# Kernel tuning notes

Measured on AMD Instinct MI355X. Metric: run time of the kernel, lower is better.

The kernel has to match this reference:

```python
import jax, jax.numpy as jnp
import numpy as np

H = 256      # hidden_dim
NH = 8       # num_heads
D = H // NH  # per-head dim
NEG = -(2.0**32) + 1.0
EPS = 1e-5


def setup_inputs() -> dict:
    key = jax.random.key(0)
    ks = jax.random.split(key, 12)
    N, Tq, Tk = 2, 2048, 2048
    s = 1.0 / np.sqrt(H)
    return {
        "Q": jax.random.normal(ks[0], (N, Tq, H), jnp.float32),
        "K": jax.random.normal(ks[1], (N, Tk, H), jnp.float32),
        "V": jax.random.normal(ks[2], (N, Tk, H), jnp.float32),
        "Wq": jax.random.normal(ks[3], (H, H), jnp.float32) * s,
        "bq": jnp.zeros((H,), jnp.float32),
        "Wk": jax.random.normal(ks[4], (H, H), jnp.float32) * s,
        "bk": jnp.zeros((H,), jnp.float32),
        "Wv": jax.random.normal(ks[5], (H, H), jnp.float32) * s,
        "bv": jnp.zeros((H,), jnp.float32),
        "gamma": jnp.ones((H,), jnp.float32),
        "beta": jnp.zeros((H,), jnp.float32),
    }


def _split_heads(x):
    # [N,T,H] -> [h,N,T,D]  (matches torch split(dim=2)+cat(dim=0): head-major)
    N, T, _ = x.shape
    return x.reshape(N, T, NH, D).transpose(2, 0, 1, 3)


def reference(Q, K, V, Wq, bq, Wk, bk, Wv, bv, gamma, beta):
    N, Tq, _ = Q.shape
    Tk = K.shape[1]
    Ql = jax.nn.relu(Q @ Wq + bq)
    Kl = jax.nn.relu(K @ Wk + bk)
    Vl = jax.nn.relu(V @ Wv + bv)
    Qh, Kh, Vh = _split_heads(Ql), _split_heads(Kl), _split_heads(Vl)

    scores = jnp.einsum("hnqd,hnkd->hnqk", Qh, Kh) / jnp.sqrt(jnp.float32(D))
    key_mask = jnp.sign(jnp.abs(K).sum(-1))    # [N,Tk]
    scores = jnp.where(key_mask[None, :, None, :] == 0, NEG, scores)
    attn = jax.nn.softmax(scores / 0.01, axis=-1)
    query_mask = jnp.sign(jnp.abs(Q).sum(-1))  # [N,Tq]
    attn = attn * query_mask[None, :, :, None]  # dropout p=0 -> identity

    ctx = jnp.einsum("hnqk,hnkd->hnqd", attn[..., :-1], Vh[:, :, :-1, :])
    out = ctx.transpose(1, 2, 0, 3).reshape(N, Tq, H)

    mu = out.mean(-1, keepdims=True)
    var = ((out - mu) ** 2).mean(-1, keepdims=True)
    out = (out - mu) / jnp.sqrt(var + EPS) * gamma + beta

    weight = attn.transpose(1, 2, 0, 3).reshape(N, Tq, NH * Tk).mean(-1)
    return out, weight
```

## Files before the change

kernel.cpp:

```cpp
#include <hip/hip_runtime.h>
#include <math.h>

#define H_DIM 256
#define NHEAD 8
#define DHEAD 32
#define NB 2
#define TSEQ 2048
#define LN_EPS 1e-5f

#define QK2_SCALE 25.503486f
#define SPLIT 4
#define TILES_PER (TSEQ / 64 / SPLIT)

typedef _Float16 half8 __attribute__((ext_vector_type(8)));
typedef _Float16 half4t __attribute__((ext_vector_type(4)));
typedef _Float16 half2t __attribute__((ext_vector_type(2)));
typedef float f32x4 __attribute__((ext_vector_type(4)));

__device__ __forceinline__ f32x4 mfma16(half8 a, half8 b, f32x4 c) {
  return __builtin_amdgcn_mfma_f32_16x16x32_f16(a, b, c, 0, 0, 0);
}
__device__ __forceinline__ float exp2fast(float x) {
  return __builtin_amdgcn_exp2f(x);
}
__device__ __forceinline__ half2t pkrtz(float a, float b) {
  return __builtin_bit_cast(half2t, __builtin_amdgcn_cvt_pkrtz(a, b));
}

__global__ __launch_bounds__(256) void mask_kernel(
    const float* __restrict__ Q, const float* __restrict__ K,
    float* __restrict__ qmask, float* __restrict__ kmask) {
  const int wid = threadIdx.x >> 6, lane = threadIdx.x & 63;
  int row = blockIdx.x * 4 + wid;
  const int total_q = NB * TSEQ;
  const float* src;
  float* dst;
  if (row < total_q) { src = Q + (size_t)row * H_DIM; dst = qmask + row; }
  else               { src = K + (size_t)(row - total_q) * H_DIM; dst = kmask + (row - total_q); }
  float4 v = *(const float4*)(src + lane * 4);
  float s = fabsf(v.x) + fabsf(v.y) + fabsf(v.z) + fabsf(v.w);
  #pragma unroll
  for (int off = 32; off > 0; off >>= 1) s += __shfl_xor(s, off);
  if (lane == 0) *dst = (s != 0.0f) ? 1.0f : 0.0f;
}

__global__ __launch_bounds__(256) void prepack_kernel(
    const float* __restrict__ Wq, const float* __restrict__ Wk, const float* __restrict__ Wv,
    const float* __restrict__ kmask,
    half8* __restrict__ WpkHi, half8* __restrict__ WpkLo, half8* __restrict__ AmaskF) {
  if (blockIdx.x >= 96) {
    int slot2 = (blockIdx.x - 96) * 256 + threadIdx.x;
    int n = slot2 >> 12;
    int rem = slot2 & 4095;
    int tile = rem >> 7;
    int c = (rem >> 6) & 1;
    int lane = rem & 63;
    int quad = lane >> 4, l15 = lane & 15;
    half8 am;
    #pragma unroll
    for (int j = 0; j < 8; ++j)
      am[j] = (l15 == 0) ? (_Float16)kmask[(size_t)n * TSEQ + tile * 64 + c * 32 + quad * 8 + j]
                         : (_Float16)0.0f;
    AmaskF[(((size_t)n * 32 + tile) * 2 + c) * 64 + lane] = am;
    return;
  }
  int slot = blockIdx.x * 256 + threadIdx.x;
  int lane = slot & 63;
  int fg = (slot >> 6) & 15;
  int s  = (slot >> 10) & 7;
  int which = slot >> 13;
  const float* W = which == 0 ? Wq : which == 1 ? Wk : Wv;
  int j  = fg * 16 + (lane & 15);
  int kb = s * 32 + (lane >> 4) * 8;
  half8 hi, lo;
  #pragma unroll
  for (int jj = 0; jj < 8; ++jj) {
    float x = W[(size_t)(kb + jj) * H_DIM + j];
    _Float16 h = (_Float16)x;
    hi[jj] = h;
    lo[jj] = (_Float16)(x - (float)h);
  }
  WpkHi[slot] = hi;
  WpkLo[slot] = lo;
}

__global__ __launch_bounds__(256) void proj_kernel(
    const float* __restrict__ Q, const float* __restrict__ K, const float* __restrict__ V,
    const float* __restrict__ bq, const float* __restrict__ bk, const float* __restrict__ bv,
    const half8* __restrict__ WpkHi, const half8* __restrict__ WpkLo,
    const float* __restrict__ kmask,
    half8* __restrict__ Gqhi, half8* __restrict__ Gqlo,
    half8* __restrict__ Gkhi, half8* __restrict__ Gklo, half8* __restrict__ Gv) {
  const int which = blockIdx.z;
  const float* X    = which == 0 ? Q  : which == 1 ? K  : V;
  const float* bias = which == 0 ? bq : which == 1 ? bk : bv;

  __shared__ __align__(16) float T[64 * 68];

  const int tid = threadIdx.x;
  const int w = tid >> 6, lane = tid & 63;
  const int l15 = lane & 15, quad = lane >> 4;
  const int mbase = blockIdx.y * 64;
  const int nfg   = blockIdx.x * 4;
  const int nn   = mbase >> 11;
  const int tile = blockIdx.y & 31;

  half8 ahi[8], alo[8];
  {
    const float* xrow = X + (size_t)(mbase + w * 16 + l15) * H_DIM + quad * 8;
    #pragma unroll
    for (int s = 0; s < 8; ++s) {
      float4 a0 = *(const float4*)(xrow + s * 32);
      float4 a1 = *(const float4*)(xrow + s * 32 + 4);
      float xs[8] = {a0.x, a0.y, a0.z, a0.w, a1.x, a1.y, a1.z, a1.w};
      #pragma unroll
      for (int i = 0; i < 8; ++i) {
        _Float16 h = (_Float16)xs[i];
        ahi[s][i] = h;
        alo[s][i] = (_Float16)(xs[i] - (float)h);
      }
    }
  }

  f32x4 acc[4];
  #pragma unroll
  for (int f = 0; f < 4; ++f) acc[f] = (f32x4){0.f, 0.f, 0.f, 0.f};

  #pragma unroll
  for (int s = 0; s < 8; ++s) {
    const half8* ph = WpkHi + (((size_t)which * 8 + s) * 16 + nfg) * 64 + lane;
    const half8* pl = WpkLo + (((size_t)which * 8 + s) * 16 + nfg) * 64 + lane;
    #pragma unroll
    for (int f = 0; f < 4; ++f) {
      half8 BH = ph[f * 64];
      half8 BL = pl[f * 64];
      acc[f] = mfma16(ahi[s], BH, acc[f]);
      acc[f] = mfma16(ahi[s], BL, acc[f]);
      acc[f] = mfma16(alo[s], BH, acc[f]);
    }
  }

  #pragma unroll
  for (int f = 0; f < 4; ++f) {
    float bj = bias[blockIdx.x * 64 + f * 16 + l15];
    #pragma unroll
    for (int r = 0; r < 4; ++r) {
      int row = w * 16 + quad * 4 + r;
      float val = fmaxf(acc[f][r] + bj, 0.0f);
      if (which == 2 && ((mbase + row) & (TSEQ - 1)) == TSEQ - 1) val = 0.0f;
      T[row * 68 + f * 16 + l15] = val;
    }
  }
  __syncthreads();

  if (which < 2) {
    const int fq = tid >> 6, lp = tid & 63;
    const int kdc = lp >> 4, krlo = lp & 15;
    const int row = fq * 16 + krlo;
    const float sc = (which == 0) ? QK2_SCALE : 1.0f;
    #pragma unroll
    for (int hs = 0; hs < 2; ++hs) {
      const float* p = &T[row * 68 + hs * 32 + kdc * 8];
      float4 a0 = *(const float4*)p;
      float4 a1 = *(const float4*)(p + 4);
      float xs[8] = {a0.x, a0.y, a0.z, a0.w, a1.x, a1.y, a1.z, a1.w};
      half8 hi, lo;
      #pragma unroll
      for (int i = 0; i < 8; ++i) {
        float x = xs[i] * sc;
        _Float16 h = (_Float16)x;
        hi[i] = h;
        lo[i] = (_Float16)(x - (float)h);
      }
      int hn = (blockIdx.x * 2 + hs) * NB + nn;
      size_t di = ((size_t)hn * 32 + tile) * 256 + tid;
      if (which == 0) { Gqhi[di] = hi; Gqlo[di] = lo; }
      else            { Gkhi[di] = hi; Gklo[di] = lo; }
    }
  } else {
    const int top = tid >> 6, mid = (tid >> 4) & 3, low = tid & 15;
    const int c = top >> 1, hh = top & 1;
    const int trow0 = (c * 4 + mid) * 8;
    float km[8];
    #pragma unroll
    for (int j = 0; j < 8; ++j)
      km[j] = kmask[(size_t)nn * TSEQ + tile * 64 + trow0 + j];
    #pragma unroll
    for (int hs = 0; hs < 2; ++hs) {
      const int col = hs * 32 + hh * 16 + low;
      half8 v8;
      #pragma unroll
      for (int j = 0; j < 8; ++j)
        v8[j] = (_Float16)(T[(trow0 + j) * 68 + col] * km[j]);
      int hn = (blockIdx.x * 2 + hs) * NB + nn;
      Gv[((size_t)hn * 32 + tile) * 256 + tid] = v8;
    }
  }
}

__global__ __launch_bounds__(256) void attn_kernel(
    const half8* __restrict__ Gqhi, const half8* __restrict__ Gqlo,
    const half8* __restrict__ Gkhi, const half8* __restrict__ Gklo,
    const half8* __restrict__ Gv, const half8* __restrict__ AmaskF,
    _Float16* __restrict__ Opf, float* __restrict__ Mp, float* __restrict__ Lp) {
  __shared__ __align__(16) half8 Vf[2][256];
  __shared__ __align__(16) _Float16 Pbuf[4][16][72];

  const int tid = threadIdx.x;
  const int w = tid >> 6, lane = tid & 63;
  const int l15 = lane & 15, quad = lane >> 4;

  const int b = blockIdx.x;
  const int g    = ((b & 7) << 1) | ((b >> 3) & 1);
  const int qt   = (b >> 4) & 31;
  const int sblk = b >> 9;
  const int n = g & 1;

  const size_t fbase = (size_t)g * 32 * 256;
  const int tile0 = sblk * TILES_PER;

  half8 qhi = Gqhi[fbase + (size_t)qt * 256 + w * 64 + lane];
  half8 qlo = Gqlo[fbase + (size_t)qt * 256 + w * 64 + lane];

  float m_q = -1.0e30f;
  f32x4 O0, O1, Ol;
  O0 = (f32x4){0.f, 0.f, 0.f, 0.f};
  O1 = (f32x4){0.f, 0.f, 0.f, 0.f};
  Ol = (f32x4){0.f, 0.f, 0.f, 0.f};

  const half8* kh  = Gkhi + fbase + (size_t)tile0 * 256 + lane;
  const half8* kl  = Gklo + fbase + (size_t)tile0 * 256 + lane;
  const half8* gv  = Gv   + fbase + (size_t)tile0 * 256 + tid;
  const half8* amp = AmaskF + (((size_t)n * 32 + tile0) * 2) * 64 + lane;

  half8 KH[4], KL[4];
  #pragma unroll
  for (int f = 0; f < 4; ++f) { KH[f] = kh[f * 64]; KL[f] = kl[f * 64]; }
  Vf[0][tid] = gv[0];

  #pragma unroll
  for (int tt = 0; tt < TILES_PER; ++tt) {
    half8 KHn[4], KLn[4], vnext;
    if (tt < TILES_PER - 1) {
      #pragma unroll
      for (int f = 0; f < 4; ++f) { KHn[f] = kh[256 + f * 64]; KLn[f] = kl[256 + f * 64]; }
      vnext = gv[256];
    }
    half8 am0 = amp[0];
    half8 am1 = amp[64];

    __syncthreads();
    if (tt < TILES_PER - 1)
      Vf[(tt + 1) & 1][tid] = vnext;

    f32x4 S[4];
    #pragma unroll
    for (int f = 0; f < 4; ++f) {
      f32x4 a = (f32x4){0.f, 0.f, 0.f, 0.f};
      a = mfma16(KL[f], qhi, a);
      a = mfma16(KH[f], qlo, a);
      a = mfma16(KH[f], qhi, a);
      S[f] = a;
    }

    float t0 = fmaxf(fmaxf(S[0][0], S[0][1]), fmaxf(S[0][2], S[0][3]));
    float t1 = fmaxf(fmaxf(S[1][0], S[1][1]), fmaxf(S[1][2], S[1][3]));
    float t2 = fmaxf(fmaxf(S[2][0], S[2][1]), fmaxf(S[2][2], S[2][3]));
    float t3 = fmaxf(fmaxf(S[3][0], S[3][1]), fmaxf(S[3][2], S[3][3]));
    float mx = fmaxf(fmaxf(t0, t1), fmaxf(t2, t3));
    mx = fmaxf(mx, __shfl_xor(mx, 16));
    mx = fmaxf(mx, __shfl_xor(mx, 32));

    float mnew = fmaxf(m_q, mx);
    float alpha = exp2fast(m_q - mnew);
    m_q = mnew;

    #pragma unroll
    for (int f = 0; f < 4; ++f) {
      float p0 = exp2fast(S[f][0] - m_q);
      float p1 = exp2fast(S[f][1] - m_q);
      float p2 = exp2fast(S[f][2] - m_q);
      float p3 = exp2fast(S[f][3] - m_q);
      half2t a01 = pkrtz(p0, p1);
      half2t a23 = pkrtz(p2, p3);
      *(half2t*)&Pbuf[w][l15][f * 16 + quad * 4]     = a01;
      *(half2t*)&Pbuf[w][l15][f * 16 + quad * 4 + 2] = a23;
    }
    #pragma unroll
    for (int r = 0; r < 4; ++r) { O0[r] *= alpha; O1[r] *= alpha; }
    Ol[0] *= alpha;
    asm volatile("s_waitcnt lgkmcnt(0)" ::: "memory");

    const half8* vbuf = (const half8*)Vf[tt & 1];
    #pragma unroll
    for (int c = 0; c < 2; ++c) {
      half8 pb = *(const half8*)&Pbuf[w][l15][c * 32 + quad * 8];
      O0 = mfma16(vbuf[(c * 2 + 0) * 64 + lane], pb, O0);
      O1 = mfma16(vbuf[(c * 2 + 1) * 64 + lane], pb, O1);
      Ol = mfma16(c == 0 ? am0 : am1, pb, Ol);
    }

    #pragma unroll
    for (int f = 0; f < 4; ++f) { KH[f] = KHn[f]; KL[f] = KLn[f]; }
    kh += 256; kl += 256; gv += 256; amp += 128;
  }

  {
    int q = qt * 64 + w * 16 + l15;
    size_t idx = ((size_t)(sblk * 16 + g) * TSEQ + q) * DHEAD;
    half4t o0 = {(_Float16)O0[0], (_Float16)O0[1], (_Float16)O0[2], (_Float16)O0[3]};
    half4t o1 = {(_Float16)O1[0], (_Float16)O1[1], (_Float16)O1[2], (_Float16)O1[3]};
    *(half4t*)&Opf[idx + quad * 4]      = o0;
    *(half4t*)&Opf[idx + 16 + quad * 4] = o1;
    if (quad == 0) {
      Mp[(size_t)(sblk * 16 + g) * TSEQ + q] = m_q;
      Lp[(size_t)(sblk * 16 + g) * TSEQ + q] = Ol[0];
    }
  }
}

__global__ __launch_bounds__(256) void ln_kernel(
    const _Float16* __restrict__ Opf, const float* __restrict__ Mp, const float* __restrict__ Lp,
    const float* __restrict__ gamma, const float* __restrict__ beta,
    const float* __restrict__ qmask,
    float* __restrict__ out, float* __restrict__ wout) {
  const int wid = threadIdx.x >> 6, lane = threadIdx.x & 63;
  const int row = blockIdx.x * 4 + wid;
  const int n = row >> 11, q = row & (TSEQ - 1);
  const int hh = lane >> 3;
  const int hn = hh * NB + n;
  const int dbase = (lane & 7) * 4;

  float m[SPLIT], l[SPLIT];
  half4t P[SPLIT];
  #pragma unroll
  for (int i = 0; i < SPLIT; ++i) {
    size_t si = (size_t)(i * 16 + hn) * TSEQ + q;
    P[i] = *(const half4t*)&Opf[si * DHEAD + dbase];
    m[i] = Mp[si];
    l[i] = Lp[si];
  }
  float mm = fmaxf(fmaxf(m[0], m[1]), fmaxf(m[2], m[3]));
  float denom = 0.f;
  float a[SPLIT];
  #pragma unroll
  for (int i = 0; i < SPLIT; ++i) { a[i] = exp2fast(m[i] - mm); denom += l[i] * a[i]; }
  float qm = qmask[row];
  float inv = qm / denom;

  float4 x = make_float4(0.f, 0.f, 0.f, 0.f);
  #pragma unroll
  for (int i = 0; i < SPLIT; ++i) {
    x.x += (float)P[i][0] * a[i]; x.y += (float)P[i][1] * a[i];
    x.z += (float)P[i][2] * a[i]; x.w += (float)P[i][3] * a[i];
  }
  x.x *= inv; x.y *= inv; x.z *= inv; x.w *= inv;

  float s = x.x + x.y + x.z + x.w;
  #pragma unroll
  for (int off = 32; off > 0; off >>= 1) s += __shfl_xor(s, off);
  float mu = s * (1.0f / H_DIM);
  float dx0 = x.x - mu, dx1 = x.y - mu, dx2 = x.z - mu, dx3 = x.w - mu;
  float sq = dx0 * dx0 + dx1 * dx1 + dx2 * dx2 + dx3 * dx3;
  #pragma unroll
  for (int off = 32; off > 0; off >>= 1) sq += __shfl_xor(sq, off);
  float rstd = rsqrtf(sq * (1.0f / H_DIM) + LN_EPS);
  float4 g = *(const float4*)(gamma + lane * 4);
  float4 bb = *(const float4*)(beta + lane * 4);
  float4 y;
  y.x = dx0 * rstd * g.x + bb.x;
  y.y = dx1 * rstd * g.y + bb.y;
  y.z = dx2 * rstd * g.z + bb.z;
  y.w = dx3 * rstd * g.w + bb.w;
  *(float4*)(out + (size_t)row * H_DIM + lane * 4) = y;
  if (lane == 0) wout[row] = qm * (1.0f / TSEQ);
}

extern "C" void kernel_launch(void* const* d_in, const int* in_sizes, int n_in,
                              void* d_out, int out_size, void* d_ws, size_t ws_size,
                              hipStream_t stream) {
  const float* Q  = (const float*)d_in[0];
  const float* K  = (const float*)d_in[1];
  const float* V  = (const float*)d_in[2];
  const float* Wq = (const float*)d_in[3];
  const float* bq = (const float*)d_in[4];
  const float* Wk = (const float*)d_in[5];
  const float* bk = (const float*)d_in[6];
  const float* Wv = (const float*)d_in[7];
  const float* bv = (const float*)d_in[8];
  const float* gamma = (const float*)d_in[9];
  const float* beta  = (const float*)d_in[10];

  char* ws = (char*)d_ws;
  const size_t NFRAG = (size_t)16 * 32 * 256;
  _Float16* Opf = (_Float16*)ws;
  half8* Gqhi = (half8*)(ws + (size_t)SPLIT * 16 * TSEQ * DHEAD * 2);
  half8* Gqlo = Gqhi + NFRAG;
  half8* Gkhi = Gqlo + NFRAG;
  half8* Gklo = Gkhi + NFRAG;
  half8* Gv   = Gklo + NFRAG;
  float* Mp = (float*)(Gv + NFRAG);
  float* Lp = Mp + SPLIT * 16 * TSEQ;
  float* qmask = Lp + SPLIT * 16 * TSEQ;
  float* kmask = qmask + NB * TSEQ;
  half8* WpkHi = (half8*)(kmask + NB * TSEQ);
  half8* WpkLo = WpkHi + 24576;
  half8* AmaskF = WpkLo + 24576;

  float* out  = (float*)d_out;
  float* wout = out + (size_t)NB * TSEQ * H_DIM;

  hipLaunchKernelGGL(mask_kernel, dim3(2 * NB * TSEQ / 4), dim3(256), 0, stream,
                     Q, K, qmask, kmask);
  hipLaunchKernelGGL(prepack_kernel, dim3(128), dim3(256), 0, stream,
                     Wq, Wk, Wv, kmask, WpkHi, WpkLo, AmaskF);
  hipLaunchKernelGGL(proj_kernel, dim3(H_DIM / 64, NB * TSEQ / 64, 3), dim3(256), 0, stream,
                     Q, K, V, bq, bk, bv, WpkHi, WpkLo, kmask,
                     Gqhi, Gqlo, Gkhi, Gklo, Gv);
  hipLaunchKernelGGL(attn_kernel, dim3(16 * 32 * SPLIT), dim3(256), 0, stream,
                     Gqhi, Gqlo, Gkhi, Gklo, Gv, AmaskF, Opf, Mp, Lp);
  hipLaunchKernelGGL(ln_kernel, dim3(NB * TSEQ / 4), dim3(256), 0, stream,
                     Opf, Mp, Lp, gamma, beta, qmask, out, wout);
}
```

Before: 131.8 us.

## Drop LDS V staging and register prefetch; read K/V directly from global

The attention kernel no longer stages V tiles through a double-buffered shared-memory array with a per-tile __syncthreads. Each wave now loads its V fragments straight from global memory (likely L2-resident) inside the PV mfma loop. The explicit next-tile register prefetch of K hi/lo fragments is also removed, so K is loaded just before use. This cuts LDS traffic, barriers and register pressure, but each wave now fetches V redundantly and loses the software prefetch that hid global-load latency.

Result: slower. 136.5 us (+3.6%).

```diff
diff --git a/kernel.cpp b/kernel.cpp
--- a/kernel.cpp
+++ b/kernel.cpp
@@ -203,7 +203,6 @@
     const half8* __restrict__ Gkhi, const half8* __restrict__ Gklo,
     const half8* __restrict__ Gv, const half8* __restrict__ AmaskF,
     _Float16* __restrict__ Opf, float* __restrict__ Mp, float* __restrict__ Lp) {
-  __shared__ __align__(16) half8 Vf[2][256];
   __shared__ __align__(16) _Float16 Pbuf[4][16][72];
 
   const int tid = threadIdx.x;
@@ -230,38 +229,24 @@
 
   const half8* kh  = Gkhi + fbase + (size_t)tile0 * 256 + lane;
   const half8* kl  = Gklo + fbase + (size_t)tile0 * 256 + lane;
-  const half8* gv  = Gv   + fbase + (size_t)tile0 * 256 + tid;
+  const half8* gv  = Gv   + fbase + (size_t)tile0 * 256 + lane;
   const half8* amp = AmaskF + (((size_t)n * 32 + tile0) * 2) * 64 + lane;
 
-  half8 KH[4], KL[4];
-  #pragma unroll
-  for (int f = 0; f < 4; ++f) { KH[f] = kh[f * 64]; KL[f] = kl[f * 64]; }
-  Vf[0][tid] = gv[0];
-
   #pragma unroll
   for (int tt = 0; tt < TILES_PER; ++tt) {
-    half8 KHn[4], KLn[4], vnext;
-    if (tt < TILES_PER - 1) {
-      #pragma unroll
-      for (int f = 0; f < 4; ++f) { KHn[f] = kh[256 + f * 64]; KLn[f] = kl[256 + f * 64]; }
-      vnext = gv[256];
+    f32x4 S[4];
+    #pragma unroll
+    for (int f = 0; f < 4; ++f) {
+      half8 KH = kh[f * 64];
+      half8 KL = kl[f * 64];
+      f32x4 a = (f32x4){0.f, 0.f, 0.f, 0.f};
+      a = mfma16(KL, qhi, a);
+      a = mfma16(KH, qlo, a);
+      a = mfma16(KH, qhi, a);
+      S[f] = a;
     }
     half8 am0 = amp[0];
     half8 am1 = amp[64];
-
-    __syncthreads();
-    if (tt < TILES_PER - 1)
-      Vf[(tt + 1) & 1][tid] = vnext;
-
-    f32x4 S[4];
-    #pragma unroll
-    for (int f = 0; f < 4; ++f) {
-      f32x4 a = (f32x4){0.f, 0.f, 0.f, 0.f};
-      a = mfma16(KL[f], qhi, a);
-      a = mfma16(KH[f], qlo, a);
-      a = mfma16(KH[f], qhi, a);
-      S[f] = a;
-    }
 
     float t0 = fmaxf(fmaxf(S[0][0], S[0][1]), fmaxf(S[0][2], S[0][3]));
     float t1 = fmaxf(fmaxf(S[1][0], S[1][1]), fmaxf(S[1][2], S[1][3]));
@@ -291,17 +276,14 @@
     Ol[0] *= alpha;
     asm volatile("s_waitcnt lgkmcnt(0)" ::: "memory");
 
-    const half8* vbuf = (const half8*)Vf[tt & 1];
     #pragma unroll
     for (int c = 0; c < 2; ++c) {
       half8 pb = *(const half8*)&Pbuf[w][l15][c * 32 + quad * 8];
-      O0 = mfma16(vbuf[(c * 2 + 0) * 64 + lane], pb, O0);
-      O1 = mfma16(vbuf[(c * 2 + 1) * 64 + lane], pb, O1);
+      O0 = mfma16(gv[(c * 2 + 0) * 64], pb, O0);
+      O1 = mfma16(gv[(c * 2 + 1) * 64], pb, O1);
       Ol = mfma16(c == 0 ? am0 : am1, pb, Ol);
     }
 
-    #pragma unroll
-    for (int f = 0; f < 4; ++f) { KH[f] = KHn[f]; KL[f] = KLn[f]; }
     kh += 256; kl += 256; gv += 256; amp += 128;
   }
 
```

## Process two query tiles per attention block to reuse K/V fragments

Applied to the files above, without the earlier changes.

Each attention block now handles two 64-row query tiles instead of one, so every K and V fragment loaded is used for twice as many MFMAs. The grid is halved to match. Register prefetching of the next K tile is dropped, with K loaded directly inside the loop. This cuts global K traffic and V LDS staging per query. In exchange the block count drops to 1024, register pressure rises and the load latency is no longer hidden by prefetch.

New measurement: 134.8 us. 2.3% more time.

```diff
diff --git a/kernel.cpp b/kernel.cpp
--- a/kernel.cpp
+++ b/kernel.cpp
@@ -204,7 +204,7 @@
     const half8* __restrict__ Gv, const half8* __restrict__ AmaskF,
     _Float16* __restrict__ Opf, float* __restrict__ Mp, float* __restrict__ Lp) {
   __shared__ __align__(16) half8 Vf[2][256];
-  __shared__ __align__(16) _Float16 Pbuf[4][16][72];
+  __shared__ __align__(16) _Float16 Pbuf[4][32][72];
 
   const int tid = threadIdx.x;
   const int w = tid >> 6, lane = tid & 63;
@@ -212,40 +212,33 @@
 
   const int b = blockIdx.x;
   const int g    = ((b & 7) << 1) | ((b >> 3) & 1);
-  const int qt   = (b >> 4) & 31;
-  const int sblk = b >> 9;
+  const int qt   = (b >> 4) & 15;
+  const int sblk = b >> 8;
   const int n = g & 1;
 
   const size_t fbase = (size_t)g * 32 * 256;
   const int tile0 = sblk * TILES_PER;
 
-  half8 qhi = Gqhi[fbase + (size_t)qt * 256 + w * 64 + lane];
-  half8 qlo = Gqlo[fbase + (size_t)qt * 256 + w * 64 + lane];
-
-  float m_q = -1.0e30f;
-  f32x4 O0, O1, Ol;
-  O0 = (f32x4){0.f, 0.f, 0.f, 0.f};
-  O1 = (f32x4){0.f, 0.f, 0.f, 0.f};
-  Ol = (f32x4){0.f, 0.f, 0.f, 0.f};
+  half8 qhi0 = Gqhi[fbase + (size_t)(qt * 2 + 0) * 256 + w * 64 + lane];
+  half8 qlo0 = Gqlo[fbase + (size_t)(qt * 2 + 0) * 256 + w * 64 + lane];
+  half8 qhi1 = Gqhi[fbase + (size_t)(qt * 2 + 1) * 256 + w * 64 + lane];
+  half8 qlo1 = Gqlo[fbase + (size_t)(qt * 2 + 1) * 256 + w * 64 + lane];
+
+  float m_q0 = -1.0e30f, m_q1 = -1.0e30f;
+  f32x4 O00, O01, Ol0, O10, O11, Ol1;
+  O00 = O01 = Ol0 = O10 = O11 = Ol1 = (f32x4){0.f, 0.f, 0.f, 0.f};
 
   const half8* kh  = Gkhi + fbase + (size_t)tile0 * 256 + lane;
   const half8* kl  = Gklo + fbase + (size_t)tile0 * 256 + lane;
   const half8* gv  = Gv   + fbase + (size_t)tile0 * 256 + tid;
   const half8* amp = AmaskF + (((size_t)n * 32 + tile0) * 2) * 64 + lane;
 
-  half8 KH[4], KL[4];
-  #pragma unroll
-  for (int f = 0; f < 4; ++f) { KH[f] = kh[f * 64]; KL[f] = kl[f * 64]; }
   Vf[0][tid] = gv[0];
 
   #pragma unroll
   for (int tt = 0; tt < TILES_PER; ++tt) {
-    half8 KHn[4], KLn[4], vnext;
-    if (tt < TILES_PER - 1) {
-      #pragma unroll
-      for (int f = 0; f < 4; ++f) { KHn[f] = kh[256 + f * 64]; KLn[f] = kl[256 + f * 64]; }
-      vnext = gv[256];
-    }
+    half8 vnext;
+    if (tt < TILES_PER - 1) vnext = gv[256];
     half8 am0 = amp[0];
     half8 am1 = amp[64];
 
@@ -253,68 +246,110 @@
     if (tt < TILES_PER - 1)
       Vf[(tt + 1) & 1][tid] = vnext;
 
-    f32x4 S[4];
+    f32x4 S0[4], S1[4];
     #pragma unroll
     for (int f = 0; f < 4; ++f) {
-      f32x4 a = (f32x4){0.f, 0.f, 0.f, 0.f};
-      a = mfma16(KL[f], qhi, a);
-      a = mfma16(KH[f], qlo, a);
-      a = mfma16(KH[f], qhi, a);
-      S[f] = a;
-    }
-
-    float t0 = fmaxf(fmaxf(S[0][0], S[0][1]), fmaxf(S[0][2], S[0][3]));
-    float t1 = fmaxf(fmaxf(S[1][0], S[1][1]), fmaxf(S[1][2], S[1][3]));
-    float t2 = fmaxf(fmaxf(S[2][0], S[2][1]), fmaxf(S[2][2], S[2][3]));
-    float t3 = fmaxf(fmaxf(S[3][0], S[3][1]), fmaxf(S[3][2], S[3][3]));
-    float mx = fmaxf(fmaxf(t0, t1), fmaxf(t2, t3));
-    mx = fmaxf(mx, __shfl_xor(mx, 16));
-    mx = fmaxf(mx, __shfl_xor(mx, 32));
-
-    float mnew = fmaxf(m_q, mx);
-    float alpha = exp2fast(m_q - mnew);
-    m_q = mnew;
-
-    #pragma unroll
-    for (int f = 0; f < 4; ++f) {
-      float p0 = exp2fast(S[f][0] - m_q);
-      float p1 = exp2fast(S[f][1] - m_q);
-      float p2 = exp2fast(S[f][2] - m_q);
-      float p3 = exp2fast(S[f][3] - m_q);
-      half2t a01 = pkrtz(p0, p1);
-      half2t a23 = pkrtz(p2, p3);
-      *(half2t*)&Pbuf[w][l15][f * 16 + quad * 4]     = a01;
-      *(half2t*)&Pbuf[w][l15][f * 16 + quad * 4 + 2] = a23;
-    }
-    #pragma unroll
-    for (int r = 0; r < 4; ++r) { O0[r] *= alpha; O1[r] *= alpha; }
-    Ol[0] *= alpha;
+      half8 KH = kh[f * 64];
+      half8 KL = kl[f * 64];
+      f32x4 a0 = (f32x4){0.f, 0.f, 0.f, 0.f};
+      a0 = mfma16(KL, qhi0, a0);
+      a0 = mfma16(KH, qlo0, a0);
+      a0 = mfma16(KH, qhi0, a0);
+      S0[f] = a0;
+      f32x4 a1 = (f32x4){0.f, 0.f, 0.f, 0.f};
+      a1 = mfma16(KL, qhi1, a1);
+      a1 = mfma16(KH, qlo1, a1);
+      a1 = mfma16(KH, qhi1, a1);
+      S1[f] = a1;
+    }
+
+    {
+      float t0 = fmaxf(fmaxf(S0[0][0], S0[0][1]), fmaxf(S0[0][2], S0[0][3]));
+      float t1 = fmaxf(fmaxf(S0[1][0], S0[1][1]), fmaxf(S0[1][2], S0[1][3]));
+      float t2 = fmaxf(fmaxf(S0[2][0], S0[2][1]), fmaxf(S0[2][2], S0[2][3]));
+      float t3 = fmaxf(fmaxf(S0[3][0], S0[3][1]), fmaxf(S0[3][2], S0[3][3]));
+      float mx = fmaxf(fmaxf(t0, t1), fmaxf(t2, t3));
+      mx = fmaxf(mx, __shfl_xor(mx, 16));
+      mx = fmaxf(mx, __shfl_xor(mx, 32));
+      float mnew = fmaxf(m_q0, mx);
+      float alpha = exp2fast(m_q0 - mnew);
+      m_q0 = mnew;
+      #pragma unroll
+      for (int f = 0; f < 4; ++f) {
+        float p0 = exp2fast(S0[f][0] - m_q0);
+        float p1 = exp2fast(S0[f][1] - m_q0);
+        float p2 = exp2fast(S0[f][2] - m_q0);
+        float p3 = exp2fast(S0[f][3] - m_q0);
+        *(half2t*)&Pbuf[w][l15][f * 16 + quad * 4]     = pkrtz(p0, p1);
+        *(half2t*)&Pbuf[w][l15][f * 16 + quad * 4 + 2] = pkrtz(p2, p3);
+      }
+      #pragma unroll
+      for (int r = 0; r < 4; ++r) { O00[r] *= alpha; O01[r] *= alpha; }
+      Ol0[0] *= alpha;
+    }
+    {
+      float t0 = fmaxf(fmaxf(S1[0][0], S1[0][1]), fmaxf(S1[0][2], S1[0][3]));
+      float t1 = fmaxf(fmaxf(S1[1][0], S1[1][1]), fmaxf(S1[1][2], S1[1][3]));
+      float t2 = fmaxf(fmaxf(S1[2][0], S1[2][1]), fmaxf(S1[2][2], S1[2][3]));
+      float t3 = fmaxf(fmaxf(S1[3][0], S1[3][1]), fmaxf(S1[3][2], S1[3][3]));
+      float mx = fmaxf(fmaxf(t0, t1), fmaxf(t2, t3));
+      mx = fmaxf(mx, __shfl_xor(mx, 16));
+      mx = fmaxf(mx, __shfl_xor(mx, 32));
+      float mnew = fmaxf(m_q1, mx);
+      float alpha = exp2fast(m_q1 - mnew);
+      m_q1 = mnew;
+      #pragma unroll
+      for (int f = 0; f < 4; ++f) {
+        float p0 = exp2fast(S1[f][0] - m_q1);
+        float p1 = exp2fast(S1[f][1] - m_q1);
+        float p2 = exp2fast(S1[f][2] - m_q1);
+        float p3 = exp2fast(S1[f][3] - m_q1);
+        *(half2t*)&Pbuf[w][16 + l15][f * 16 + quad * 4]     = pkrtz(p0, p1);
+        *(half2t*)&Pbuf[w][16 + l15][f * 16 + quad * 4 + 2] = pkrtz(p2, p3);
+      }
+      #pragma unroll
+      for (int r = 0; r < 4; ++r) { O10[r] *= alpha; O11[r] *= alpha; }
+      Ol1[0] *= alpha;
+    }
     asm volatile("s_waitcnt lgkmcnt(0)" ::: "memory");
 
     const half8* vbuf = (const half8*)Vf[tt & 1];
     #pragma unroll
     for (int c = 0; c < 2; ++c) {
-      half8 pb = *(const half8*)&Pbuf[w][l15][c * 32 + quad * 8];
-      O0 = mfma16(vbuf[(c * 2 + 0) * 64 + lane], pb, O0);
-      O1 = mfma16(vbuf[(c * 2 + 1) * 64 + lane], pb, O1);
-      Ol = mfma16(c == 0 ? am0 : am1, pb, Ol);
-    }
-
-    #pragma unroll
-    for (int f = 0; f < 4; ++f) { KH[f] = KHn[f]; KL[f] = KLn[f]; }
+      half8 vA = vbuf[(c * 2 + 0) * 64 + lane];
+      half8 vB = vbuf[(c * 2 + 1) * 64 + lane];
+      half8 amc = (c == 0) ? am0 : am1;
+      half8 pb0 = *(const half8*)&Pbuf[w][l15][c * 32 + quad * 8];
+      half8 pb1 = *(const half8*)&Pbuf[w][16 + l15][c * 32 + quad * 8];
+      O00 = mfma16(vA, pb0, O00);
+      O01 = mfma16(vB, pb0, O01);
+      Ol0 = mfma16(amc, pb0, Ol0);
+      O10 = mfma16(vA, pb1, O10);
+      O11 = mfma16(vB, pb1, O11);
+      Ol1 = mfma16(amc, pb1, Ol1);
+    }
+
     kh += 256; kl += 256; gv += 256; amp += 128;
   }
 
   {
-    int q = qt * 64 + w * 16 + l15;
-    size_t idx = ((size_t)(sblk * 16 + g) * TSEQ + q) * DHEAD;
-    half4t o0 = {(_Float16)O0[0], (_Float16)O0[1], (_Float16)O0[2], (_Float16)O0[3]};
-    half4t o1 = {(_Float16)O1[0], (_Float16)O1[1], (_Float16)O1[2], (_Float16)O1[3]};
-    *(half4t*)&Opf[idx + quad * 4]      = o0;
-    *(half4t*)&Opf[idx + 16 + quad * 4] = o1;
+    int q0 = qt * 128 + w * 16 + l15;
+    size_t base = (size_t)(sblk * 16 + g) * TSEQ;
+    size_t i0 = (base + q0) * DHEAD;
+    size_t i1 = (base + q0 + 64) * DHEAD;
+    half4t a0 = {(_Float16)O00[0], (_Float16)O00[1], (_Float16)O00[2], (_Float16)O00[3]};
+    half4t a1 = {(_Float16)O01[0], (_Float16)O01[1], (_Float16)O01[2], (_Float16)O01[3]};
+    half4t b0 = {(_Float16)O10[0], (_Float16)O10[1], (_Float16)O10[2], (_Float16)O10[3]};
+    half4t b1 = {(_Float16)O11[0], (_Float16)O11[1], (_Float16)O11[2], (_Float16)O11[3]};
+    *(half4t*)&Opf[i0 + quad * 4]      = a0;
+    *(half4t*)&Opf[i0 + 16 + quad * 4] = a1;
+    *(half4t*)&Opf[i1 + quad * 4]      = b0;
+    *(half4t*)&Opf[i1 + 16 + quad * 4] = b1;
     if (quad == 0) {
-      Mp[(size_t)(sblk * 16 + g) * TSEQ + q] = m_q;
-      Lp[(size_t)(sblk * 16 + g) * TSEQ + q] = Ol[0];
+      Mp[base + q0]      = m_q0;
+      Lp[base + q0]      = Ol0[0];
+      Mp[base + q0 + 64] = m_q1;
+      Lp[base + q0 + 64] = Ol1[0];
     }
   }
 }
@@ -417,7 +452,7 @@
   hipLaunchKernelGGL(proj_kernel, dim3(H_DIM / 64, NB * TSEQ / 64, 3), dim3(256), 0, stream,
                      Q, K, V, bq, bk, bv, WpkHi, WpkLo, kmask,
                      Gqhi, Gqlo, Gkhi, Gklo, Gv);
-  hipLaunchKernelGGL(attn_kernel, dim3(16 * 32 * SPLIT), dim3(256), 0, stream,
+  hipLaunchKernelGGL(attn_kernel, dim3(16 * 16 * SPLIT), dim3(256), 0, stream,
                      Gqhi, Gqlo, Gkhi, Gklo, Gv, AmaskF, Opf, Mp, Lp);
   hipLaunchKernelGGL(ln_kernel, dim3(NB * TSEQ / 4), dim3(256), 0, stream,
                      Opf, Mp, Lp, gamma, beta, qmask, out, wout);
```

## Fold mask computation into prepack and layernorm kernels, apply key mask in attention

Applied to the files above, without the earlier changes.

Removes the standalone mask kernel. The key mask is now computed inside extra blocks of the prepack kernel, and the query mask is recomputed from raw Q inside the layernorm kernel. The key mask is no longer folded into V and no longer precomputed as an A-fragment. Instead the attention kernel multiplies the exponentiated scores by the key mask directly and sums the row with a constant ones fragment, which saves one launch and the mask-fragment buffers at the cost of extra loads and multiplies in the attention loop.

Measured after the change: 131.9 us. Within noise of the previous version (+0.1%).

```diff
diff --git a/kernel.cpp b/kernel.cpp
--- a/kernel.cpp
+++ b/kernel.cpp
@@ -27,41 +27,18 @@
   return __builtin_bit_cast(half2t, __builtin_amdgcn_cvt_pkrtz(a, b));
 }
 
-__global__ __launch_bounds__(256) void mask_kernel(
-    const float* __restrict__ Q, const float* __restrict__ K,
-    float* __restrict__ qmask, float* __restrict__ kmask) {
-  const int wid = threadIdx.x >> 6, lane = threadIdx.x & 63;
-  int row = blockIdx.x * 4 + wid;
-  const int total_q = NB * TSEQ;
-  const float* src;
-  float* dst;
-  if (row < total_q) { src = Q + (size_t)row * H_DIM; dst = qmask + row; }
-  else               { src = K + (size_t)(row - total_q) * H_DIM; dst = kmask + (row - total_q); }
-  float4 v = *(const float4*)(src + lane * 4);
-  float s = fabsf(v.x) + fabsf(v.y) + fabsf(v.z) + fabsf(v.w);
-  #pragma unroll
-  for (int off = 32; off > 0; off >>= 1) s += __shfl_xor(s, off);
-  if (lane == 0) *dst = (s != 0.0f) ? 1.0f : 0.0f;
-}
-
 __global__ __launch_bounds__(256) void prepack_kernel(
     const float* __restrict__ Wq, const float* __restrict__ Wk, const float* __restrict__ Wv,
-    const float* __restrict__ kmask,
-    half8* __restrict__ WpkHi, half8* __restrict__ WpkLo, half8* __restrict__ AmaskF) {
+    const float* __restrict__ Kraw,
+    half8* __restrict__ WpkHi, half8* __restrict__ WpkLo, float* __restrict__ kmask) {
   if (blockIdx.x >= 96) {
-    int slot2 = (blockIdx.x - 96) * 256 + threadIdx.x;
-    int n = slot2 >> 12;
-    int rem = slot2 & 4095;
-    int tile = rem >> 7;
-    int c = (rem >> 6) & 1;
-    int lane = rem & 63;
-    int quad = lane >> 4, l15 = lane & 15;
-    half8 am;
-    #pragma unroll
-    for (int j = 0; j < 8; ++j)
-      am[j] = (l15 == 0) ? (_Float16)kmask[(size_t)n * TSEQ + tile * 64 + c * 32 + quad * 8 + j]
-                         : (_Float16)0.0f;
-    AmaskF[(((size_t)n * 32 + tile) * 2 + c) * 64 + lane] = am;
+    const int wid = threadIdx.x >> 6, lane = threadIdx.x & 63;
+    int row = (blockIdx.x - 96) * 4 + wid;
+    float4 v = *(const float4*)(Kraw + (size_t)row * H_DIM + lane * 4);
+    float s = fabsf(v.x) + fabsf(v.y) + fabsf(v.z) + fabsf(v.w);
+    #pragma unroll
+    for (int off = 32; off > 0; off >>= 1) s += __shfl_xor(s, off);
+    if (lane == 0) kmask[row] = (s != 0.0f) ? 1.0f : 0.0f;
     return;
   }
   int slot = blockIdx.x * 256 + threadIdx.x;
@@ -88,7 +65,6 @@
     const float* __restrict__ Q, const float* __restrict__ K, const float* __restrict__ V,
     const float* __restrict__ bq, const float* __restrict__ bk, const float* __restrict__ bv,
     const half8* __restrict__ WpkHi, const half8* __restrict__ WpkLo,
-    const float* __restrict__ kmask,
     half8* __restrict__ Gqhi, half8* __restrict__ Gqlo,
     half8* __restrict__ Gkhi, half8* __restrict__ Gklo, half8* __restrict__ Gv) {
   const int which = blockIdx.z;
@@ -181,17 +157,13 @@
     const int top = tid >> 6, mid = (tid >> 4) & 3, low = tid & 15;
     const int c = top >> 1, hh = top & 1;
     const int trow0 = (c * 4 + mid) * 8;
-    float km[8];
-    #pragma unroll
-    for (int j = 0; j < 8; ++j)
-      km[j] = kmask[(size_t)nn * TSEQ + tile * 64 + trow0 + j];
     #pragma unroll
     for (int hs = 0; hs < 2; ++hs) {
       const int col = hs * 32 + hh * 16 + low;
       half8 v8;
       #pragma unroll
       for (int j = 0; j < 8; ++j)
-        v8[j] = (_Float16)(T[(trow0 + j) * 68 + col] * km[j]);
+        v8[j] = (_Float16)T[(trow0 + j) * 68 + col];
       int hn = (blockIdx.x * 2 + hs) * NB + nn;
       Gv[((size_t)hn * 32 + tile) * 256 + tid] = v8;
     }
@@ -201,7 +173,7 @@
 __global__ __launch_bounds__(256) void attn_kernel(
     const half8* __restrict__ Gqhi, const half8* __restrict__ Gqlo,
     const half8* __restrict__ Gkhi, const half8* __restrict__ Gklo,
-    const half8* __restrict__ Gv, const half8* __restrict__ AmaskF,
+    const half8* __restrict__ Gv, const float* __restrict__ kmask,
     _Float16* __restrict__ Opf, float* __restrict__ Mp, float* __restrict__ Lp) {
   __shared__ __align__(16) half8 Vf[2][256];
   __shared__ __align__(16) _Float16 Pbuf[4][16][72];
@@ -222,6 +194,10 @@
   half8 qhi = Gqhi[fbase + (size_t)qt * 256 + w * 64 + lane];
   half8 qlo = Gqlo[fbase + (size_t)qt * 256 + w * 64 + lane];
 
+  half8 onesA;
+  #pragma unroll
+  for (int i = 0; i < 8; ++i) onesA[i] = (l15 == 0) ? (_Float16)1.0f : (_Float16)0.0f;
+
   float m_q = -1.0e30f;
   f32x4 O0, O1, Ol;
   O0 = (f32x4){0.f, 0.f, 0.f, 0.f};
@@ -231,7 +207,7 @@
   const half8* kh  = Gkhi + fbase + (size_t)tile0 * 256 + lane;
   const half8* kl  = Gklo + fbase + (size_t)tile0 * 256 + lane;
   const half8* gv  = Gv   + fbase + (size_t)tile0 * 256 + tid;
-  const half8* amp = AmaskF + (((size_t)n * 32 + tile0) * 2) * 64 + lane;
+  const float* kmp = kmask + (size_t)n * TSEQ + tile0 * 64 + quad * 4;
 
   half8 KH[4], KL[4];
   #pragma unroll
@@ -246,8 +222,9 @@
       for (int f = 0; f < 4; ++f) { KHn[f] = kh[256 + f * 64]; KLn[f] = kl[256 + f * 64]; }
       vnext = gv[256];
     }
-    half8 am0 = amp[0];
-    half8 am1 = amp[64];
+    float4 km[4];
+    #pragma unroll
+    for (int f = 0; f < 4; ++f) km[f] = *(const float4*)(kmp + tt * 64 + f * 16);
 
     __syncthreads();
     if (tt < TILES_PER - 1)
@@ -277,14 +254,12 @@
 
     #pragma unroll
     for (int f = 0; f < 4; ++f) {
-      float p0 = exp2fast(S[f][0] - m_q);
-      float p1 = exp2fast(S[f][1] - m_q);
-      float p2 = exp2fast(S[f][2] - m_q);
-      float p3 = exp2fast(S[f][3] - m_q);
-      half2t a01 = pkrtz(p0, p1);
-      half2t a23 = pkrtz(p2, p3);
-      *(half2t*)&Pbuf[w][l15][f * 16 + quad * 4]     = a01;
-      *(half2t*)&Pbuf[w][l15][f * 16 + quad * 4 + 2] = a23;
+      float p0 = exp2fast(S[f][0] - m_q) * km[f].x;
+      float p1 = exp2fast(S[f][1] - m_q) * km[f].y;
+      float p2 = exp2fast(S[f][2] - m_q) * km[f].z;
+      float p3 = exp2fast(S[f][3] - m_q) * km[f].w;
+      *(half2t*)&Pbuf[w][l15][f * 16 + quad * 4]     = pkrtz(p0, p1);
+      *(half2t*)&Pbuf[w][l15][f * 16 + quad * 4 + 2] = pkrtz(p2, p3);
     }
     #pragma unroll
     for (int r = 0; r < 4; ++r) { O0[r] *= alpha; O1[r] *= alpha; }
@@ -297,12 +272,12 @@
       half8 pb = *(const half8*)&Pbuf[w][l15][c * 32 + quad * 8];
       O0 = mfma16(vbuf[(c * 2 + 0) * 64 + lane], pb, O0);
       O1 = mfma16(vbuf[(c * 2 + 1) * 64 + lane], pb, O1);
-      Ol = mfma16(c == 0 ? am0 : am1, pb, Ol);
+      Ol = mfma16(onesA, pb, Ol);
     }
 
     #pragma unroll
     for (int f = 0; f < 4; ++f) { KH[f] = KHn[f]; KL[f] = KLn[f]; }
-    kh += 256; kl += 256; gv += 256; amp += 128;
+    kh += 256; kl += 256; gv += 256;
   }
 
   {
@@ -322,7 +297,7 @@
 __global__ __launch_bounds__(256) void ln_kernel(
     const _Float16* __restrict__ Opf, const float* __restrict__ Mp, const float* __restrict__ Lp,
     const float* __restrict__ gamma, const float* __restrict__ beta,
-    const float* __restrict__ qmask,
+    const float* __restrict__ Qraw,
     float* __restrict__ out, float* __restrict__ wout) {
   const int wid = threadIdx.x >> 6, lane = threadIdx.x & 63;
   const int row = blockIdx.x * 4 + wid;
@@ -331,6 +306,12 @@
   const int hn = hh * NB + n;
   const int dbase = (lane & 7) * 4;
 
+  float4 qv = *(const float4*)(Qraw + (size_t)row * H_DIM + lane * 4);
+  float qs = fabsf(qv.x) + fabsf(qv.y) + fabsf(qv.z) + fabsf(qv.w);
+  #pragma unroll
+  for (int off = 32; off > 0; off >>= 1) qs += __shfl_xor(qs, off);
+  float qm = (qs != 0.0f) ? 1.0f : 0.0f;
+
   float m[SPLIT], l[SPLIT];
   half4t P[SPLIT];
   #pragma unroll
@@ -345,7 +326,6 @@
   float a[SPLIT];
   #pragma unroll
   for (int i = 0; i < SPLIT; ++i) { a[i] = exp2fast(m[i] - mm); denom += l[i] * a[i]; }
-  float qm = qmask[row];
   float inv = qm / denom;
 
   float4 x = make_float4(0.f, 0.f, 0.f, 0.f);
@@ -401,24 +381,20 @@
   half8* Gv   = Gklo + NFRAG;
   float* Mp = (float*)(Gv + NFRAG);
   float* Lp = Mp + SPLIT * 16 * TSEQ;
-  float* qmask = Lp + SPLIT * 16 * TSEQ;
-  float* kmask = qmask + NB * TSEQ;
+  float* kmask = Lp + SPLIT * 16 * TSEQ;
   half8* WpkHi = (half8*)(kmask + NB * TSEQ);
   half8* WpkLo = WpkHi + 24576;
-  half8* AmaskF = WpkLo + 24576;
 
   float* out  = (float*)d_out;
   float* wout = out + (size_t)NB * TSEQ * H_DIM;
 
-  hipLaunchKernelGGL(mask_kernel, dim3(2 * NB * TSEQ / 4), dim3(256), 0, stream,
-                     Q, K, qmask, kmask);
-  hipLaunchKernelGGL(prepack_kernel, dim3(128), dim3(256), 0, stream,
-                     Wq, Wk, Wv, kmask, WpkHi, WpkLo, AmaskF);
+  hipLaunchKernelGGL(prepack_kernel, dim3(96 + NB * TSEQ / 4), dim3(256), 0, stream,
+                     Wq, Wk, Wv, K, WpkHi, WpkLo, kmask);
   hipLaunchKernelGGL(proj_kernel, dim3(H_DIM / 64, NB * TSEQ / 64, 3), dim3(256), 0, stream,
-                     Q, K, V, bq, bk, bv, WpkHi, WpkLo, kmask,
+                     Q, K, V, bq, bk, bv, WpkHi, WpkLo,
                      Gqhi, Gqlo, Gkhi, Gklo, Gv);
   hipLaunchKernelGGL(attn_kernel, dim3(16 * 32 * SPLIT), dim3(256), 0, stream,
-                     Gqhi, Gqlo, Gkhi, Gklo, Gv, AmaskF, Opf, Mp, Lp);
+                     Gqhi, Gqlo, Gkhi, Gklo, Gv, kmask, Opf, Mp, Lp);
   hipLaunchKernelGGL(ln_kernel, dim3(NB * TSEQ / 4), dim3(256), 0, stream,
-                     Opf, Mp, Lp, gamma, beta, qmask, out, wout);
-}
+                     Opf, Mp, Lp, gamma, beta, Q, out, wout);
+}
```
